# Kernel optimization log

Hardware: AMD Instinct MI355X
Metric: run time of the kernel (lower is better)

Reference implementation:

```python
import jax, jax.numpy as jnp
import numpy as np
import math

DIM = 1024
NUM_HEADS = 16
HEAD_DIM = DIM // NUM_HEADS
SCALE = HEAD_DIM ** -0.5
WINDOW_SIZE = 256
IS_SLIDING = True
IS_CAUSAL = True


def _alibi_slopes(num_heads: int) -> np.ndarray:
    closest_pow2 = 2 ** math.floor(math.log2(num_heads))
    base = 2.0 ** (-2.0 ** (-(math.log2(closest_pow2) - 3)))
    powers = np.arange(1, closest_pow2 + 1, dtype=np.float32)
    slopes = base ** powers
    if num_heads != closest_pow2:
        start = 2.0 ** (-(2.0 ** (-(math.log2(closest_pow2) - 3)) - 1))
        extra = np.linspace(start, base, num_heads - closest_pow2, dtype=np.float32)
        slopes = np.concatenate([slopes, extra])
    return slopes.astype(np.float32)


def setup_inputs() -> dict:
    key = jax.random.key(0)
    k_x, k_qw, k_qb, k_pw, k_pb = jax.random.split(key, 5)
    B, N, C = 2, 2048, DIM
    s = C ** -0.5
    return {
        "x": jax.random.normal(k_x, (B, N, C), dtype=jnp.float32),
        "qkv_w": jax.random.normal(k_qw, (3 * C, C), dtype=jnp.float32) * s,
        "qkv_b": jax.random.normal(k_qb, (3 * C,), dtype=jnp.float32) * 0.02,
        "proj_w": jax.random.normal(k_pw, (C, C), dtype=jnp.float32) * s,
        "proj_b": jax.random.normal(k_pb, (C,), dtype=jnp.float32) * 0.02,
    }


def reference(x, qkv_w, qkv_b, proj_w, proj_b):
    B, N, C = x.shape
    H, D = NUM_HEADS, HEAD_DIM
    slopes = jnp.asarray(_alibi_slopes(H))  # [H]

    qkv = x @ qkv_w.T + qkv_b                         # [B,N,3C]
    qkv = qkv.reshape(B, N, 3, H, D).transpose(2, 0, 3, 1, 4)  # [3,B,H,N,D]
    q, k, v = qkv[0], qkv[1], qkv[2]

    attn = jnp.einsum('bhnd,bhmd->bhnm', q, k) * SCALE  # [B,H,N,N]

    pos = jnp.arange(N)
    rel = pos[None, :] - pos[:, None]                  # rel[i,j] = j - i
    # alibi = slope*|rel|, negated where rel<0  ==  slope*rel
    alibi = slopes[:, None, None] * rel.astype(jnp.float32)   # [H,N,N]
    attn = attn + alibi[None]

    if IS_SLIDING:
        attn = jnp.where(jnp.abs(rel) >= WINDOW_SIZE, -jnp.inf, attn)
    if IS_CAUSAL:
        attn = jnp.where(rel > 0, -jnp.inf, attn)      # mask strictly-upper triangle

    attn = jax.nn.softmax(attn, axis=-1)
    out = jnp.einsum('bhnm,bhmd->bhnd', attn, v)       # [B,H,N,D]
    out = out.transpose(0, 2, 1, 3).reshape(B, N, C)
    return out @ proj_w.T + proj_b
```

## Files before the change

### kernel.cpp

```cpp
#include <hip/hip_runtime.h>
#include <hip/hip_bf16.h>
#include <cmath>

#define B_ 2
#define N_ 2048
#define C_ 1024
#define H_ 16
#define D_ 64
#define BHND (B_*H_*N_*D_)

typedef __attribute__((ext_vector_type(8))) short  bf16x8;
typedef __attribute__((ext_vector_type(4))) float  f32x4;
typedef __attribute__((ext_vector_type(4))) unsigned int uint4v;
typedef __attribute__((ext_vector_type(2))) unsigned int uint2v;

__device__ __forceinline__ unsigned pack_hi2(float x0, float x1) {
  return __builtin_amdgcn_perm(__float_as_uint(x1), __float_as_uint(x0), 0x07060302u);
}
__device__ __forceinline__ float trunc16(float x) {
  return __uint_as_float(__float_as_uint(x) & 0xFFFF0000u);
}
__device__ __forceinline__ void cvt8(const float4 u, const float4 v,
                                     uint4v& hi, uint4v& lo) {
  hi.x = pack_hi2(u.x, u.y); hi.y = pack_hi2(u.z, u.w);
  hi.z = pack_hi2(v.x, v.y); hi.w = pack_hi2(v.z, v.w);
  float l0 = u.x - trunc16(u.x), l1 = u.y - trunc16(u.y);
  float l2 = u.z - trunc16(u.z), l3 = u.w - trunc16(u.w);
  float l4 = v.x - trunc16(v.x), l5 = v.y - trunc16(v.y);
  float l6 = v.z - trunc16(v.z), l7 = v.w - trunc16(v.w);
  lo.x = pack_hi2(l0, l1); lo.y = pack_hi2(l2, l3);
  lo.z = pack_hi2(l4, l5); lo.w = pack_hi2(l6, l7);
}
__device__ __forceinline__ int swz(int row, int kelem) {
  return ((row << 7) + (kelem << 1)) ^ ((row & 7) << 4);
}

template<int MODE>
__global__ __launch_bounds__(256, 2)
void gemm3_nt(const float* __restrict__ A, const float* __restrict__ Bw,
              const float* __restrict__ bias, float* __restrict__ Cd,
              int Ncols, int K)
{
  __shared__ char smem[65536];
  char* Ah = smem;          char* Al = smem + 16384;
  char* Bh = smem + 32768;  char* Bl = smem + 49152;

  const int t    = threadIdx.x;
  const int lane = t & 63;
  const int w    = t >> 6;
  const int wm   = w >> 1, wn = w & 1;
  const int mb   = blockIdx.x, nb = blockIdx.y;

  const int srow = t >> 1;
  const int skh  = (t & 1) * 32;
  const float* Ag = A  + (size_t)(mb*128 + srow)*K + skh;
  const float* Bg = Bw + (size_t)(nb*128 + srow)*K + skh;

  f32x4 acc[4][4];
  #pragma unroll
  for (int m = 0; m < 4; ++m)
    #pragma unroll
    for (int n = 0; n < 4; ++n) acc[m][n] = (f32x4)0.f;

  float4 fa[8], fb[8];
  {
    const float4* ap = (const float4*)Ag;
    const float4* bp = (const float4*)Bg;
    #pragma unroll
    for (int i = 0; i < 8; ++i) { fa[i] = ap[i]; fb[i] = bp[i]; }
  }

  const int fr = lane & 15;
  const int fg = lane >> 4;
  const int nkt = K / 64;

  for (int kt = 0; kt < nkt; ++kt) {
    __syncthreads();
    #pragma unroll
    for (int cc = 0; cc < 4; ++cc) {
      uint4v hi, lo;
      const int off = swz(srow, skh + cc*8);
      cvt8(fa[2*cc], fa[2*cc+1], hi, lo);
      *(uint4v*)(Ah + off) = hi;  *(uint4v*)(Al + off) = lo;
      cvt8(fb[2*cc], fb[2*cc+1], hi, lo);
      *(uint4v*)(Bh + off) = hi;  *(uint4v*)(Bl + off) = lo;
    }
    __syncthreads();
    if (kt + 1 < nkt) {
      const float4* ap = (const float4*)(Ag + (kt+1)*64);
      const float4* bp = (const float4*)(Bg + (kt+1)*64);
      #pragma unroll
      for (int i = 0; i < 8; ++i) { fa[i] = ap[i]; fb[i] = bp[i]; }
    }
    #pragma unroll
    for (int ks = 0; ks < 2; ++ks) {
      const int ke = ks*32 + fg*8;
      bf16x8 ah[4], al[4];
      #pragma unroll
      for (int m = 0; m < 4; ++m) {
        const int off = swz(wm*64 + m*16 + fr, ke);
        ah[m] = *(const bf16x8*)(Ah + off);
        al[m] = *(const bf16x8*)(Al + off);
      }
      #pragma unroll
      for (int n = 0; n < 4; ++n) {
        const int off = swz(wn*64 + n*16 + fr, ke);
        const bf16x8 bh = *(const bf16x8*)(Bh + off);
        const bf16x8 bl = *(const bf16x8*)(Bl + off);
        #pragma unroll
        for (int m = 0; m < 4; ++m) {
          acc[m][n] = __builtin_amdgcn_mfma_f32_16x16x32_bf16(ah[m], bh, acc[m][n], 0, 0, 0);
          acc[m][n] = __builtin_amdgcn_mfma_f32_16x16x32_bf16(al[m], bh, acc[m][n], 0, 0, 0);
          acc[m][n] = __builtin_amdgcn_mfma_f32_16x16x32_bf16(ah[m], bl, acc[m][n], 0, 0, 0);
        }
      }
    }
  }

  #pragma unroll
  for (int n = 0; n < 4; ++n) {
    const int col = nb*128 + wn*64 + n*16 + fr;
    const float bb = bias[col];
    int which = 0, hh = 0, dd = 0;
    if (MODE == 1) { which = col >> 10; hh = (col >> 6) & 15; dd = col & 63; }
    #pragma unroll
    for (int m = 0; m < 4; ++m) {
      const int row0 = mb*128 + wm*64 + m*16 + fg*4;
      #pragma unroll
      for (int j = 0; j < 4; ++j) {
        const int row = row0 + j;
        const float val = acc[m][n][j] + bb;
        if (MODE == 0) {
          Cd[(size_t)row*Ncols + col] = val;
        } else {
          const int b = row >> 11, i = row & 2047;
          Cd[(size_t)which*BHND + (((size_t)(b*H_ + hh))*N_ + i)*D_ + dd] = val;
        }
      }
    }
  }
}

__global__ __launch_bounds__(256, 2)
void attn_mfma(const float* __restrict__ qkv, float* __restrict__ attn_out)
{
  __shared__ char smem[65536];
  char* Qh = smem;
  char* Ql = smem + 8192;
  char* Kh = smem + 16384;
  char* Kl = smem + 24576;
  char* Vh = smem + 32768;
  char* Vl = smem + 40960;
  char* Ph = smem + 49152;
  char* Pl = smem + 57344;

  const int t    = threadIdx.x;
  const int lane = t & 63;
  const int w    = t >> 6;
  const int g    = lane >> 4;
  const int c    = lane & 15;
  const int qt   = blockIdx.x & 31;
  const int bh   = blockIdx.x >> 5;
  const int h    = bh & 15;
  const int b    = bh >> 4;

  const float* qg = qkv + (size_t)bh*N_*D_;
  const float* kg = qg + (size_t)BHND;
  const float* vg = kg + (size_t)BHND;

  const float slope = exp2f(-0.5f*(float)(h+1));
  const int kt0 = max(0, qt - 4);
  const int ktN = qt;

  const int srow = t >> 2;
  const int scq  = (t & 3) * 16;
  const int vkey = t & 63;
  const int vdb  = (t >> 6) * 16;

  {
    const float4* qp = (const float4*)(qg + (size_t)(qt*64 + srow)*D_ + scq);
    float4 q0=qp[0], q1=qp[1], q2=qp[2], q3=qp[3];
    const float4* kp = (const float4*)(kg + (size_t)(kt0*64 + srow)*D_ + scq);
    float4 k0=kp[0], k1=kp[1], k2=kp[2], k3=kp[3];
    const float4* vp = (const float4*)(vg + (size_t)(kt0*64 + vkey)*D_ + vdb);
    float4 v0=vp[0], v1=vp[1], v2=vp[2], v3=vp[3];
    uint4v hi, lo;
    cvt8(q0,q1,hi,lo); *(uint4v*)(Qh+swz(srow,scq  ))=hi; *(uint4v*)(Ql+swz(srow,scq  ))=lo;
    cvt8(q2,q3,hi,lo); *(uint4v*)(Qh+swz(srow,scq+8))=hi; *(uint4v*)(Ql+swz(srow,scq+8))=lo;
    cvt8(k0,k1,hi,lo); *(uint4v*)(Kh+swz(srow,scq  ))=hi; *(uint4v*)(Kl+swz(srow,scq  ))=lo;
    cvt8(k2,k3,hi,lo); *(uint4v*)(Kh+swz(srow,scq+8))=hi; *(uint4v*)(Kl+swz(srow,scq+8))=lo;
    const float vv[16] = {v0.x,v0.y,v0.z,v0.w, v1.x,v1.y,v1.z,v1.w,
                          v2.x,v2.y,v2.z,v2.w, v3.x,v3.y,v3.z,v3.w};
    #pragma unroll
    for (int d16 = 0; d16 < 16; ++d16) {
      const int d  = vdb + d16;
      const int off = swz(d, vkey);
      const unsigned xu = __float_as_uint(vv[d16]);
      *(unsigned short*)(Vh + off) = (unsigned short)(xu >> 16);
      const float xt = __uint_as_float(xu & 0xFFFF0000u);
      *(unsigned short*)(Vl + off) = (unsigned short)(__float_as_uint(vv[d16] - xt) >> 16);
    }
  }
  __syncthreads();

  bf16x8 qbh[2], qbl[2];
  #pragma unroll
  for (int ks = 0; ks < 2; ++ks) {
    const int off = swz(w*16 + c, ks*32 + g*8);
    qbh[ks] = *(const bf16x8*)(Qh + off);
    qbl[ks] = *(const bf16x8*)(Ql + off);
  }

  float4 pk[4], pvv[4];
  if (kt0 < ktN) {
    const float4* kp = (const float4*)(kg + (size_t)((kt0+1)*64 + srow)*D_ + scq);
    const float4* vp = (const float4*)(vg + (size_t)((kt0+1)*64 + vkey)*D_ + vdb);
    #pragma unroll
    for (int i = 0; i < 4; ++i) { pk[i] = kp[i]; pvv[i] = vp[i]; }
  }

  f32x4 co[4];
  #pragma unroll
  for (int n = 0; n < 4; ++n) co[n] = (f32x4)0.f;
  float mrun = -1e20f, lrun = 0.f;
  const int iq = qt*64 + w*16 + c;
  const int pbase = w*2048;

  for (int kt = kt0; ; ++kt) {
    f32x4 sc[4];
    #pragma unroll
    for (int f = 0; f < 4; ++f) sc[f] = (f32x4)0.f;
    #pragma unroll
    for (int ks = 0; ks < 2; ++ks) {
      #pragma unroll
      for (int f = 0; f < 4; ++f) {
        const int off = swz(f*16 + c, ks*32 + g*8);
        const bf16x8 ah = *(const bf16x8*)(Kh + off);
        const bf16x8 al = *(const bf16x8*)(Kl + off);
        sc[f] = __builtin_amdgcn_mfma_f32_16x16x32_bf16(ah, qbh[ks], sc[f], 0,0,0);
        sc[f] = __builtin_amdgcn_mfma_f32_16x16x32_bf16(al, qbh[ks], sc[f], 0,0,0);
        sc[f] = __builtin_amdgcn_mfma_f32_16x16x32_bf16(ah, qbl[ks], sc[f], 0,0,0);
      }
    }
    float sv[4][4];
    float mt = -1e30f;
    #pragma unroll
    for (int f = 0; f < 4; ++f)
      #pragma unroll
      for (int r = 0; r < 4; ++r) {
        const int rel = kt*64 + f*16 + g*4 + r - iq;
        float s = fmaf(sc[f][r], 0.125f, slope*(float)rel);
        s = (rel > 0 || rel < -255) ? -1e30f : s;
        sv[f][r] = s;
        mt = fmaxf(mt, s);
      }
    mt = fmaxf(mt, __shfl_xor(mt, 16));
    mt = fmaxf(mt, __shfl_xor(mt, 32));
    const float mnew = fmaxf(mrun, mt);
    const float corr = __expf(mrun - mnew);
    mrun = mnew;
    float pw[4][4];
    float psum = 0.f;
    #pragma unroll
    for (int f = 0; f < 4; ++f)
      #pragma unroll
      for (int r = 0; r < 4; ++r) {
        const float p = __expf(sv[f][r] - mnew);
        pw[f][r] = p;
        psum += p;
      }
    psum += __shfl_xor(psum, 16);
    psum += __shfl_xor(psum, 32);
    lrun = lrun*corr + psum;
    #pragma unroll
    for (int f = 0; f < 4; ++f) {
      const int off = swz(c, f*16 + g*4);
      uint2v ph2, pl2;
      ph2.x = pack_hi2(pw[f][0], pw[f][1]);
      ph2.y = pack_hi2(pw[f][2], pw[f][3]);
      pl2.x = pack_hi2(pw[f][0]-trunc16(pw[f][0]), pw[f][1]-trunc16(pw[f][1]));
      pl2.y = pack_hi2(pw[f][2]-trunc16(pw[f][2]), pw[f][3]-trunc16(pw[f][3]));
      *(uint2v*)(Ph + pbase + off) = ph2;
      *(uint2v*)(Pl + pbase + off) = pl2;
    }
    const float c0 = __shfl(corr, g*4+0);
    const float c1 = __shfl(corr, g*4+1);
    const float c2 = __shfl(corr, g*4+2);
    const float c3 = __shfl(corr, g*4+3);
    #pragma unroll
    for (int n = 0; n < 4; ++n) {
      co[n][0] *= c0; co[n][1] *= c1; co[n][2] *= c2; co[n][3] *= c3;
    }
    #pragma unroll
    for (int ks = 0; ks < 2; ++ks) {
      const int poff = swz(c, ks*32 + g*8);
      const bf16x8 pah = *(const bf16x8*)(Ph + pbase + poff);
      const bf16x8 pal = *(const bf16x8*)(Pl + pbase + poff);
      #pragma unroll
      for (int n = 0; n < 4; ++n) {
        const int voff = swz(n*16 + c, ks*32 + g*8);
        const bf16x8 vbh = *(const bf16x8*)(Vh + voff);
        const bf16x8 vbl = *(const bf16x8*)(Vl + voff);
        co[n] = __builtin_amdgcn_mfma_f32_16x16x32_bf16(pah, vbh, co[n], 0,0,0);
        co[n] = __builtin_amdgcn_mfma_f32_16x16x32_bf16(pal, vbh, co[n], 0,0,0);
        co[n] = __builtin_amdgcn_mfma_f32_16x16x32_bf16(pah, vbl, co[n], 0,0,0);
      }
    }
    if (kt == ktN) break;
    __syncthreads();
    {
      uint4v hi, lo;
      cvt8(pk[0], pk[1], hi, lo);
      *(uint4v*)(Kh+swz(srow,scq  ))=hi; *(uint4v*)(Kl+swz(srow,scq  ))=lo;
      cvt8(pk[2], pk[3], hi, lo);
      *(uint4v*)(Kh+swz(srow,scq+8))=hi; *(uint4v*)(Kl+swz(srow,scq+8))=lo;
      const float vv[16] = {pvv[0].x,pvv[0].y,pvv[0].z,pvv[0].w,
                            pvv[1].x,pvv[1].y,pvv[1].z,pvv[1].w,
                            pvv[2].x,pvv[2].y,pvv[2].z,pvv[2].w,
                            pvv[3].x,pvv[3].y,pvv[3].z,pvv[3].w};
      #pragma unroll
      for (int d16 = 0; d16 < 16; ++d16) {
        const int d  = vdb + d16;
        const int off = swz(d, vkey);
        const unsigned xu = __float_as_uint(vv[d16]);
        *(unsigned short*)(Vh + off) = (unsigned short)(xu >> 16);
        const float xt = __uint_as_float(xu & 0xFFFF0000u);
        *(unsigned short*)(Vl + off) = (unsigned short)(__float_as_uint(vv[d16] - xt) >> 16);
      }
    }
    __syncthreads();
    if (kt + 1 < ktN) {
      const float4* kp = (const float4*)(kg + (size_t)((kt+2)*64 + srow)*D_ + scq);
      const float4* vp = (const float4*)(vg + (size_t)((kt+2)*64 + vkey)*D_ + vdb);
      #pragma unroll
      for (int i = 0; i < 4; ++i) { pk[i] = kp[i]; pvv[i] = vp[i]; }
    }
  }

  float linv[4];
  #pragma unroll
  for (int r = 0; r < 4; ++r) linv[r] = 1.f / __shfl(lrun, g*4+r);
  #pragma unroll
  for (int n = 0; n < 4; ++n)
    #pragma unroll
    for (int r = 0; r < 4; ++r) {
      const int qrow = qt*64 + w*16 + g*4 + r;
      attn_out[((size_t)b*N_ + qrow)*C_ + h*64 + n*16 + c] = co[n][r] * linv[r];
    }
}

extern "C" void kernel_launch(void* const* d_in, const int* in_sizes, int n_in,
                              void* d_out, int out_size, void* d_ws, size_t ws_size,
                              hipStream_t stream)
{
  const float* x      = (const float*)d_in[0];
  const float* qkv_w  = (const float*)d_in[1];
  const float* qkv_b  = (const float*)d_in[2];
  const float* proj_w = (const float*)d_in[3];
  const float* proj_b = (const float*)d_in[4];
  float* out  = (float*)d_out;
  float* qkv  = (float*)d_ws;
  float* attn = qkv + (size_t)3*BHND;

  gemm3_nt<1><<<dim3(32, 24), 256, 0, stream>>>(x, qkv_w, qkv_b, qkv, 3*C_, C_);
  attn_mfma<<<dim3(1024), 256, 0, stream>>>(qkv, attn);
  gemm3_nt<0><<<dim3(32, 8), 256, 0, stream>>>(attn, proj_w, proj_b, out, C_, C_);
}
```

Baseline: 285.5 us.

## Pre-split fp32 operands into bf16 hi/lo planes in global memory between stages

Adds a conversion kernel that splits x and both weight matrices into separate bf16 high and low arrays. The GEMM and attention kernels now load these pre-split arrays directly instead of converting fp32 on every tile load. The QKV projection and attention epilogues now also write split hi/lo bf16 outputs. This removes repeated in-kernel conversion work and keeps the total byte count per element the same, at the cost of three extra launches and extra passes over x and the weights. The new path only runs if the workspace is at least about 96 MiB; otherwise the old fp32 path is used.

```diff
diff --git a/kernel.cpp b/kernel.cpp
--- a/kernel.cpp
+++ b/kernel.cpp
@@ -8,11 +8,13 @@
 #define H_ 16
 #define D_ 64
 #define BHND (B_*H_*N_*D_)
+#define BNC  (B_*N_*C_)
 
 typedef __attribute__((ext_vector_type(8))) short  bf16x8;
 typedef __attribute__((ext_vector_type(4))) float  f32x4;
 typedef __attribute__((ext_vector_type(4))) unsigned int uint4v;
 typedef __attribute__((ext_vector_type(2))) unsigned int uint2v;
+typedef unsigned short ushort_t;
 
 __device__ __forceinline__ unsigned pack_hi2(float x0, float x1) {
   return __builtin_amdgcn_perm(__float_as_uint(x1), __float_as_uint(x0), 0x07060302u);
@@ -35,11 +37,29 @@
   return ((row << 7) + (kelem << 1)) ^ ((row & 7) << 4);
 }
 
+
+__global__ __launch_bounds__(256)
+void cvt_split(const float* __restrict__ in, ushort_t* __restrict__ h,
+               ushort_t* __restrict__ l, int n4)
+{
+  for (int i = blockIdx.x*256 + threadIdx.x; i < n4; i += gridDim.x*256) {
+    const float4 v = ((const float4*)in)[i];
+    uint2v hh, ll;
+    hh.x = pack_hi2(v.x, v.y); hh.y = pack_hi2(v.z, v.w);
+    ll.x = pack_hi2(v.x - trunc16(v.x), v.y - trunc16(v.y));
+    ll.y = pack_hi2(v.z - trunc16(v.z), v.w - trunc16(v.w));
+    *(uint2v*)(h + 4*(size_t)i) = hh;
+    *(uint2v*)(l + 4*(size_t)i) = ll;
+  }
+}
+
 template<int MODE>
 __global__ __launch_bounds__(256, 2)
-void gemm3_nt(const float* __restrict__ A, const float* __restrict__ Bw,
-              const float* __restrict__ bias, float* __restrict__ Cd,
-              int Ncols, int K)
+void gemm_b3(const ushort_t* __restrict__ Agh_, const ushort_t* __restrict__ Agl_,
+             const ushort_t* __restrict__ Bgh_, const ushort_t* __restrict__ Bgl_,
+             const float* __restrict__ bias, float* __restrict__ Cf,
+             ushort_t* __restrict__ Ch, ushort_t* __restrict__ Cl,
+             int Ncols, int K)
 {
   __shared__ char smem[65536];
   char* Ah = smem;          char* Al = smem + 16384;
@@ -53,8 +73,10 @@
 
   const int srow = t >> 1;
   const int skh  = (t & 1) * 32;
-  const float* Ag = A  + (size_t)(mb*128 + srow)*K + skh;
-  const float* Bg = Bw + (size_t)(nb*128 + srow)*K + skh;
+  const ushort_t* Agh = Agh_ + (size_t)(mb*128 + srow)*K + skh;
+  const ushort_t* Agl = Agl_ + (size_t)(mb*128 + srow)*K + skh;
+  const ushort_t* Bgh = Bgh_ + (size_t)(nb*128 + srow)*K + skh;
+  const ushort_t* Bgl = Bgl_ + (size_t)(nb*128 + srow)*K + skh;
 
   f32x4 acc[4][4];
   #pragma unroll
@@ -62,12 +84,13 @@
     #pragma unroll
     for (int n = 0; n < 4; ++n) acc[m][n] = (f32x4)0.f;
 
-  float4 fa[8], fb[8];
-  {
-    const float4* ap = (const float4*)Ag;
-    const float4* bp = (const float4*)Bg;
-    #pragma unroll
-    for (int i = 0; i < 8; ++i) { fa[i] = ap[i]; fb[i] = bp[i]; }
+  uint4v fah[4], fal[4], fbh[4], fbl[4];
+  #pragma unroll
+  for (int i = 0; i < 4; ++i) {
+    fah[i] = *(const uint4v*)(Agh + i*8);
+    fal[i] = *(const uint4v*)(Agl + i*8);
+    fbh[i] = *(const uint4v*)(Bgh + i*8);
+    fbl[i] = *(const uint4v*)(Bgl + i*8);
   }
 
   const int fr = lane & 15;
@@ -78,19 +101,20 @@
     __syncthreads();
     #pragma unroll
     for (int cc = 0; cc < 4; ++cc) {
-      uint4v hi, lo;
       const int off = swz(srow, skh + cc*8);
-      cvt8(fa[2*cc], fa[2*cc+1], hi, lo);
-      *(uint4v*)(Ah + off) = hi;  *(uint4v*)(Al + off) = lo;
-      cvt8(fb[2*cc], fb[2*cc+1], hi, lo);
-      *(uint4v*)(Bh + off) = hi;  *(uint4v*)(Bl + off) = lo;
+      *(uint4v*)(Ah + off) = fah[cc];  *(uint4v*)(Al + off) = fal[cc];
+      *(uint4v*)(Bh + off) = fbh[cc];  *(uint4v*)(Bl + off) = fbl[cc];
     }
     __syncthreads();
     if (kt + 1 < nkt) {
-      const float4* ap = (const float4*)(Ag + (kt+1)*64);
-      const float4* bp = (const float4*)(Bg + (kt+1)*64);
-      #pragma unroll
-      for (int i = 0; i < 8; ++i) { fa[i] = ap[i]; fb[i] = bp[i]; }
+      const int ko = (kt+1)*64;
+      #pragma unroll
+      for (int i = 0; i < 4; ++i) {
+        fah[i] = *(const uint4v*)(Agh + ko + i*8);
+        fal[i] = *(const uint4v*)(Agl + ko + i*8);
+        fbh[i] = *(const uint4v*)(Bgh + ko + i*8);
+        fbl[i] = *(const uint4v*)(Bgl + ko + i*8);
+      }
     }
     #pragma unroll
     for (int ks = 0; ks < 2; ++ks) {
@@ -117,6 +141,329 @@
     }
   }
 
+  #pragma unroll
+  for (int n = 0; n < 4; ++n) {
+    const int col = nb*128 + wn*64 + n*16 + fr;
+    const float bb = bias[col];
+    int which = 0, hh = 0, dd = 0;
+    if (MODE == 1) { which = col >> 10; hh = (col >> 6) & 15; dd = col & 63; }
+    #pragma unroll
+    for (int m = 0; m < 4; ++m) {
+      const int row0 = mb*128 + wm*64 + m*16 + fg*4;
+      #pragma unroll
+      for (int j = 0; j < 4; ++j) {
+        const int row = row0 + j;
+        const float val = acc[m][n][j] + bb;
+        if (MODE == 0) {
+          Cf[(size_t)row*Ncols + col] = val;
+        } else {
+          const int b = row >> 11, i = row & 2047;
+          const size_t idx = (size_t)which*BHND + (((size_t)(b*H_ + hh))*N_ + i)*D_ + dd;
+          Ch[idx] = (ushort_t)(__float_as_uint(val) >> 16);
+          Cl[idx] = (ushort_t)(__float_as_uint(val - trunc16(val)) >> 16);
+        }
+      }
+    }
+  }
+}
+
+__global__ __launch_bounds__(256, 2)
+void attn_b3(const ushort_t* __restrict__ qkvh, const ushort_t* __restrict__ qkvl,
+             ushort_t* __restrict__ outh, ushort_t* __restrict__ outl)
+{
+  __shared__ char smem[65536];
+  char* Qh = smem;
+  char* Ql = smem + 8192;
+  char* Kh = smem + 16384;
+  char* Kl = smem + 24576;
+  char* Vh = smem + 32768;
+  char* Vl = smem + 40960;
+  char* Ph = smem + 49152;
+  char* Pl = smem + 57344;
+
+  const int t    = threadIdx.x;
+  const int lane = t & 63;
+  const int w    = t >> 6;
+  const int g    = lane >> 4;
+  const int c    = lane & 15;
+  const int qt   = blockIdx.x & 31;
+  const int bh   = blockIdx.x >> 5;
+  const int h    = bh & 15;
+  const int b    = bh >> 4;
+
+  const ushort_t* qgh = qkvh + (size_t)bh*N_*D_;
+  const ushort_t* qgl = qkvl + (size_t)bh*N_*D_;
+  const ushort_t* kgh = qkvh + (size_t)BHND   + (size_t)bh*N_*D_;
+  const ushort_t* kgl = qkvl + (size_t)BHND   + (size_t)bh*N_*D_;
+  const ushort_t* vgh = qkvh + (size_t)2*BHND + (size_t)bh*N_*D_;
+  const ushort_t* vgl = qkvl + (size_t)2*BHND + (size_t)bh*N_*D_;
+
+  const float slope = exp2f(-0.5f*(float)(h+1));
+  const int kt0 = max(0, qt - 4);
+  const int ktN = qt;
+
+  const int srow = t >> 2;
+  const int scq  = (t & 3) * 16;
+  const int vkey = t & 63;
+  const int vdb  = (t >> 6) * 16;
+
+  {
+    const uint4v* qph = (const uint4v*)(qgh + (size_t)(qt*64 + srow)*D_ + scq);
+    const uint4v* qpl = (const uint4v*)(qgl + (size_t)(qt*64 + srow)*D_ + scq);
+    const uint4v* kph = (const uint4v*)(kgh + (size_t)(kt0*64 + srow)*D_ + scq);
+    const uint4v* kpl = (const uint4v*)(kgl + (size_t)(kt0*64 + srow)*D_ + scq);
+    const uint4v* vph = (const uint4v*)(vgh + (size_t)(kt0*64 + vkey)*D_ + vdb);
+    const uint4v* vpl = (const uint4v*)(vgl + (size_t)(kt0*64 + vkey)*D_ + vdb);
+    uint4v q0=qph[0], q1=qph[1], ql0=qpl[0], ql1=qpl[1];
+    uint4v k0=kph[0], k1=kph[1], kl0=kpl[0], kl1=kpl[1];
+    uint4v v0=vph[0], v1=vph[1], vl0=vpl[0], vl1=vpl[1];
+    *(uint4v*)(Qh+swz(srow,scq))   = q0;  *(uint4v*)(Qh+swz(srow,scq+8)) = q1;
+    *(uint4v*)(Ql+swz(srow,scq))   = ql0; *(uint4v*)(Ql+swz(srow,scq+8)) = ql1;
+    *(uint4v*)(Kh+swz(srow,scq))   = k0;  *(uint4v*)(Kh+swz(srow,scq+8)) = k1;
+    *(uint4v*)(Kl+swz(srow,scq))   = kl0; *(uint4v*)(Kl+swz(srow,scq+8)) = kl1;
+    #pragma unroll
+    for (int j = 0; j < 4; ++j) {
+      const int d0 = vdb + 2*j, d1 = vdb + 8 + 2*j;
+      unsigned wh = v0[j], wl = vl0[j];
+      *(ushort_t*)(Vh + swz(d0,   vkey)) = (ushort_t)(wh & 0xffffu);
+      *(ushort_t*)(Vh + swz(d0+1, vkey)) = (ushort_t)(wh >> 16);
+      *(ushort_t*)(Vl + swz(d0,   vkey)) = (ushort_t)(wl & 0xffffu);
+      *(ushort_t*)(Vl + swz(d0+1, vkey)) = (ushort_t)(wl >> 16);
+      wh = v1[j]; wl = vl1[j];
+      *(ushort_t*)(Vh + swz(d1,   vkey)) = (ushort_t)(wh & 0xffffu);
+      *(ushort_t*)(Vh + swz(d1+1, vkey)) = (ushort_t)(wh >> 16);
+      *(ushort_t*)(Vl + swz(d1,   vkey)) = (ushort_t)(wl & 0xffffu);
+      *(ushort_t*)(Vl + swz(d1+1, vkey)) = (ushort_t)(wl >> 16);
+    }
+  }
+  __syncthreads();
+
+  bf16x8 qbh[2], qbl[2];
+  #pragma unroll
+  for (int ks = 0; ks < 2; ++ks) {
+    const int off = swz(w*16 + c, ks*32 + g*8);
+    qbh[ks] = *(const bf16x8*)(Qh + off);
+    qbl[ks] = *(const bf16x8*)(Ql + off);
+  }
+
+  uint4v pkh[2], pkl[2], pvh[2], pvl[2];
+  if (kt0 < ktN) {
+    const uint4v* kph = (const uint4v*)(kgh + (size_t)((kt0+1)*64 + srow)*D_ + scq);
+    const uint4v* kpl = (const uint4v*)(kgl + (size_t)((kt0+1)*64 + srow)*D_ + scq);
+    const uint4v* vph = (const uint4v*)(vgh + (size_t)((kt0+1)*64 + vkey)*D_ + vdb);
+    const uint4v* vpl = (const uint4v*)(vgl + (size_t)((kt0+1)*64 + vkey)*D_ + vdb);
+    pkh[0]=kph[0]; pkh[1]=kph[1]; pkl[0]=kpl[0]; pkl[1]=kpl[1];
+    pvh[0]=vph[0]; pvh[1]=vph[1]; pvl[0]=vpl[0]; pvl[1]=vpl[1];
+  }
+
+  f32x4 co[4];
+  #pragma unroll
+  for (int n = 0; n < 4; ++n) co[n] = (f32x4)0.f;
+  float mrun = -1e20f, lrun = 0.f;
+  const int iq = qt*64 + w*16 + c;
+  const int pbase = w*2048;
+
+  for (int kt = kt0; ; ++kt) {
+    f32x4 sc[4];
+    #pragma unroll
+    for (int f = 0; f < 4; ++f) sc[f] = (f32x4)0.f;
+    #pragma unroll
+    for (int ks = 0; ks < 2; ++ks) {
+      #pragma unroll
+      for (int f = 0; f < 4; ++f) {
+        const int off = swz(f*16 + c, ks*32 + g*8);
+        const bf16x8 ah = *(const bf16x8*)(Kh + off);
+        const bf16x8 al = *(const bf16x8*)(Kl + off);
+        sc[f] = __builtin_amdgcn_mfma_f32_16x16x32_bf16(ah, qbh[ks], sc[f], 0,0,0);
+        sc[f] = __builtin_amdgcn_mfma_f32_16x16x32_bf16(al, qbh[ks], sc[f], 0,0,0);
+        sc[f] = __builtin_amdgcn_mfma_f32_16x16x32_bf16(ah, qbl[ks], sc[f], 0,0,0);
+      }
+    }
+    float sv[4][4];
+    float mt = -1e30f;
+    #pragma unroll
+    for (int f = 0; f < 4; ++f)
+      #pragma unroll
+      for (int r = 0; r < 4; ++r) {
+        const int rel = kt*64 + f*16 + g*4 + r - iq;
+        float s = fmaf(sc[f][r], 0.125f, slope*(float)rel);
+        s = (rel > 0 || rel < -255) ? -1e30f : s;
+        sv[f][r] = s;
+        mt = fmaxf(mt, s);
+      }
+    mt = fmaxf(mt, __shfl_xor(mt, 16));
+    mt = fmaxf(mt, __shfl_xor(mt, 32));
+    const float mnew = fmaxf(mrun, mt);
+    const float corr = __expf(mrun - mnew);
+    mrun = mnew;
+    float pw[4][4];
+    float psum = 0.f;
+    #pragma unroll
+    for (int f = 0; f < 4; ++f)
+      #pragma unroll
+      for (int r = 0; r < 4; ++r) {
+        const float p = __expf(sv[f][r] - mnew);
+        pw[f][r] = p;
+        psum += p;
+      }
+    psum += __shfl_xor(psum, 16);
+    psum += __shfl_xor(psum, 32);
+    lrun = lrun*corr + psum;
+    #pragma unroll
+    for (int f = 0; f < 4; ++f) {
+      const int off = swz(c, f*16 + g*4);
+      uint2v ph2, pl2;
+      ph2.x = pack_hi2(pw[f][0], pw[f][1]);
+      ph2.y = pack_hi2(pw[f][2], pw[f][3]);
+      pl2.x = pack_hi2(pw[f][0]-trunc16(pw[f][0]), pw[f][1]-trunc16(pw[f][1]));
+      pl2.y = pack_hi2(pw[f][2]-trunc16(pw[f][2]), pw[f][3]-trunc16(pw[f][3]));
+      *(uint2v*)(Ph + pbase + off) = ph2;
+      *(uint2v*)(Pl + pbase + off) = pl2;
+    }
+    const float c0 = __shfl(corr, g*4+0);
+    const float c1 = __shfl(corr, g*4+1);
+    const float c2 = __shfl(corr, g*4+2);
+    const float c3 = __shfl(corr, g*4+3);
+    #pragma unroll
+    for (int n = 0; n < 4; ++n) {
+      co[n][0] *= c0; co[n][1] *= c1; co[n][2] *= c2; co[n][3] *= c3;
+    }
+    #pragma unroll
+    for (int ks = 0; ks < 2; ++ks) {
+      const int poff = swz(c, ks*32 + g*8);
+      const bf16x8 pah = *(const bf16x8*)(Ph + pbase + poff);
+      const bf16x8 pal = *(const bf16x8*)(Pl + pbase + poff);
+      #pragma unroll
+      for (int n = 0; n < 4; ++n) {
+        const int voff = swz(n*16 + c, ks*32 + g*8);
+        const bf16x8 vbh = *(const bf16x8*)(Vh + voff);
+        const bf16x8 vbl = *(const bf16x8*)(Vl + voff);
+        co[n] = __builtin_amdgcn_mfma_f32_16x16x32_bf16(pah, vbh, co[n], 0,0,0);
+        co[n] = __builtin_amdgcn_mfma_f32_16x16x32_bf16(pal, vbh, co[n], 0,0,0);
+        co[n] = __builtin_amdgcn_mfma_f32_16x16x32_bf16(pah, vbl, co[n], 0,0,0);
+      }
+    }
+    if (kt == ktN) break;
+    __syncthreads();
+    {
+      *(uint4v*)(Kh+swz(srow,scq))   = pkh[0]; *(uint4v*)(Kh+swz(srow,scq+8)) = pkh[1];
+      *(uint4v*)(Kl+swz(srow,scq))   = pkl[0]; *(uint4v*)(Kl+swz(srow,scq+8)) = pkl[1];
+      #pragma unroll
+      for (int j = 0; j < 4; ++j) {
+        const int d0 = vdb + 2*j, d1 = vdb + 8 + 2*j;
+        unsigned wh = pvh[0][j], wl = pvl[0][j];
+        *(ushort_t*)(Vh + swz(d0,   vkey)) = (ushort_t)(wh & 0xffffu);
+        *(ushort_t*)(Vh + swz(d0+1, vkey)) = (ushort_t)(wh >> 16);
+        *(ushort_t*)(Vl + swz(d0,   vkey)) = (ushort_t)(wl & 0xffffu);
+        *(ushort_t*)(Vl + swz(d0+1, vkey)) = (ushort_t)(wl >> 16);
+        wh = pvh[1][j]; wl = pvl[1][j];
+        *(ushort_t*)(Vh + swz(d1,   vkey)) = (ushort_t)(wh & 0xffffu);
+        *(ushort_t*)(Vh + swz(d1+1, vkey)) = (ushort_t)(wh >> 16);
+        *(ushort_t*)(Vl + swz(d1,   vkey)) = (ushort_t)(wl & 0xffffu);
+        *(ushort_t*)(Vl + swz(d1+1, vkey)) = (ushort_t)(wl >> 16);
+      }
+    }
+    __syncthreads();
+    if (kt + 1 < ktN) {
+      const uint4v* kph = (const uint4v*)(kgh + (size_t)((kt+2)*64 + srow)*D_ + scq);
+      const uint4v* kpl = (const uint4v*)(kgl + (size_t)((kt+2)*64 + srow)*D_ + scq);
+      const uint4v* vph = (const uint4v*)(vgh + (size_t)((kt+2)*64 + vkey)*D_ + vdb);
+      const uint4v* vpl = (const uint4v*)(vgl + (size_t)((kt+2)*64 + vkey)*D_ + vdb);
+      pkh[0]=kph[0]; pkh[1]=kph[1]; pkl[0]=kpl[0]; pkl[1]=kpl[1];
+      pvh[0]=vph[0]; pvh[1]=vph[1]; pvl[0]=vpl[0]; pvl[1]=vpl[1];
+    }
+  }
+
+  float linv[4];
+  #pragma unroll
+  for (int r = 0; r < 4; ++r) linv[r] = 1.f / __shfl(lrun, g*4+r);
+  #pragma unroll
+  for (int n = 0; n < 4; ++n)
+    #pragma unroll
+    for (int r = 0; r < 4; ++r) {
+      const int qrow = qt*64 + w*16 + g*4 + r;
+      const float val = co[n][r] * linv[r];
+      const size_t idx = ((size_t)b*N_ + qrow)*C_ + h*64 + n*16 + c;
+      outh[idx] = (ushort_t)(__float_as_uint(val) >> 16);
+      outl[idx] = (ushort_t)(__float_as_uint(val - trunc16(val)) >> 16);
+    }
+}
+
+template<int MODE>
+__global__ __launch_bounds__(256, 2)
+void gemm3_nt(const float* __restrict__ A, const float* __restrict__ Bw,
+              const float* __restrict__ bias, float* __restrict__ Cd,
+              int Ncols, int K)
+{
+  __shared__ char smem[65536];
+  char* Ah = smem;          char* Al = smem + 16384;
+  char* Bh = smem + 32768;  char* Bl = smem + 49152;
+  const int t = threadIdx.x;
+  const int lane = t & 63;
+  const int w = t >> 6;
+  const int wm = w >> 1, wn = w & 1;
+  const int mb = blockIdx.x, nb = blockIdx.y;
+  const int srow = t >> 1;
+  const int skh  = (t & 1) * 32;
+  const float* Ag = A  + (size_t)(mb*128 + srow)*K + skh;
+  const float* Bg = Bw + (size_t)(nb*128 + srow)*K + skh;
+  f32x4 acc[4][4];
+  #pragma unroll
+  for (int m = 0; m < 4; ++m)
+    #pragma unroll
+    for (int n = 0; n < 4; ++n) acc[m][n] = (f32x4)0.f;
+  float4 fa[8], fb[8];
+  {
+    const float4* ap = (const float4*)Ag;
+    const float4* bp = (const float4*)Bg;
+    #pragma unroll
+    for (int i = 0; i < 8; ++i) { fa[i] = ap[i]; fb[i] = bp[i]; }
+  }
+  const int fr = lane & 15;
+  const int fg = lane >> 4;
+  const int nkt = K / 64;
+  for (int kt = 0; kt < nkt; ++kt) {
+    __syncthreads();
+    #pragma unroll
+    for (int cc = 0; cc < 4; ++cc) {
+      uint4v hi, lo;
+      const int off = swz(srow, skh + cc*8);
+      cvt8(fa[2*cc], fa[2*cc+1], hi, lo);
+      *(uint4v*)(Ah + off) = hi;  *(uint4v*)(Al + off) = lo;
+      cvt8(fb[2*cc], fb[2*cc+1], hi, lo);
+      *(uint4v*)(Bh + off) = hi;  *(uint4v*)(Bl + off) = lo;
+    }
+    __syncthreads();
+    if (kt + 1 < nkt) {
+      const float4* ap = (const float4*)(Ag + (kt+1)*64);
+      const float4* bp = (const float4*)(Bg + (kt+1)*64);
+      #pragma unroll
+      for (int i = 0; i < 8; ++i) { fa[i] = ap[i]; fb[i] = bp[i]; }
+    }
+    #pragma unroll
+    for (int ks = 0; ks < 2; ++ks) {
+      const int ke = ks*32 + fg*8;
+      bf16x8 ah[4], al[4];
+      #pragma unroll
+      for (int m = 0; m < 4; ++m) {
+        const int off = swz(wm*64 + m*16 + fr, ke);
+        ah[m] = *(const bf16x8*)(Ah + off);
+        al[m] = *(const bf16x8*)(Al + off);
+      }
+      #pragma unroll
+      for (int n = 0; n < 4; ++n) {
+        const int off = swz(wn*64 + n*16 + fr, ke);
+        const bf16x8 bh = *(const bf16x8*)(Bh + off);
+        const bf16x8 bl = *(const bf16x8*)(Bl + off);
+        #pragma unroll
+        for (int m = 0; m < 4; ++m) {
+          acc[m][n] = __builtin_amdgcn_mfma_f32_16x16x32_bf16(ah[m], bh, acc[m][n], 0, 0, 0);
+          acc[m][n] = __builtin_amdgcn_mfma_f32_16x16x32_bf16(al[m], bh, acc[m][n], 0, 0, 0);
+          acc[m][n] = __builtin_amdgcn_mfma_f32_16x16x32_bf16(ah[m], bl, acc[m][n], 0, 0, 0);
+        }
+      }
+    }
+  }
   #pragma unroll
   for (int n = 0; n < 4; ++n) {
     const int col = nb*128 + wn*64 + n*16 + fr;
@@ -153,30 +500,25 @@
   char* Vl = smem + 40960;
   char* Ph = smem + 49152;
   char* Pl = smem + 57344;
-
-  const int t    = threadIdx.x;
+  const int t = threadIdx.x;
   const int lane = t & 63;
-  const int w    = t >> 6;
-  const int g    = lane >> 4;
-  const int c    = lane & 15;
-  const int qt   = blockIdx.x & 31;
-  const int bh   = blockIdx.x >> 5;
-  const int h    = bh & 15;
-  const int b    = bh >> 4;
-
+  const int w = t >> 6;
+  const int g = lane >> 4;
+  const int c = lane & 15;
+  const int qt = blockIdx.x & 31;
+  const int bh = blockIdx.x >> 5;
+  const int h = bh & 15;
+  const int b = bh >> 4;
   const float* qg = qkv + (size_t)bh*N_*D_;
   const float* kg = qg + (size_t)BHND;
   const float* vg = kg + (size_t)BHND;
-
   const float slope = exp2f(-0.5f*(float)(h+1));
   const int kt0 = max(0, qt - 4);
   const int ktN = qt;
-
   const int srow = t >> 2;
   const int scq  = (t & 3) * 16;
   const int vkey = t & 63;
   const int vdb  = (t >> 6) * 16;
-
   {
     const float4* qp = (const float4*)(qg + (size_t)(qt*64 + srow)*D_ + scq);
     float4 q0=qp[0], q1=qp[1], q2=qp[2], q3=qp[3];
@@ -202,7 +544,6 @@
     }
   }
   __syncthreads();
-
   bf16x8 qbh[2], qbl[2];
   #pragma unroll
   for (int ks = 0; ks < 2; ++ks) {
@@ -210,7 +551,6 @@
     qbh[ks] = *(const bf16x8*)(Qh + off);
     qbl[ks] = *(const bf16x8*)(Ql + off);
   }
-
   float4 pk[4], pvv[4];
   if (kt0 < ktN) {
     const float4* kp = (const float4*)(kg + (size_t)((kt0+1)*64 + srow)*D_ + scq);
@@ -218,14 +558,12 @@
     #pragma unroll
     for (int i = 0; i < 4; ++i) { pk[i] = kp[i]; pvv[i] = vp[i]; }
   }
-
   f32x4 co[4];
   #pragma unroll
   for (int n = 0; n < 4; ++n) co[n] = (f32x4)0.f;
   float mrun = -1e20f, lrun = 0.f;
   const int iq = qt*64 + w*16 + c;
   const int pbase = w*2048;
-
   for (int kt = kt0; ; ++kt) {
     f32x4 sc[4];
     #pragma unroll
@@ -336,7 +674,6 @@
       for (int i = 0; i < 4; ++i) { pk[i] = kp[i]; pvv[i] = vp[i]; }
     }
   }
-
   float linv[4];
   #pragma unroll
   for (int r = 0; r < 4; ++r) linv[r] = 1.f / __shfl(lrun, g*4+r);
@@ -358,11 +695,36 @@
   const float* qkv_b  = (const float*)d_in[2];
   const float* proj_w = (const float*)d_in[3];
   const float* proj_b = (const float*)d_in[4];
-  float* out  = (float*)d_out;
-  float* qkv  = (float*)d_ws;
-  float* attn = qkv + (size_t)3*BHND;
-
-  gemm3_nt<1><<<dim3(32, 24), 256, 0, stream>>>(x, qkv_w, qkv_b, qkv, 3*C_, C_);
-  attn_mfma<<<dim3(1024), 256, 0, stream>>>(qkv, attn);
-  gemm3_nt<0><<<dim3(32, 8), 256, 0, stream>>>(attn, proj_w, proj_b, out, C_, C_);
-}
+  float* out = (float*)d_out;
+
+  const size_t NEED = 100663296;
+  if (ws_size >= NEED) {
+    ushort_t* W     = (ushort_t*)d_ws;
+    ushort_t* qkvh  = W;
+    ushort_t* qkvl  = qkvh + (size_t)3*BHND;
+    ushort_t* attnh = qkvl + (size_t)3*BHND;
+    ushort_t* attnl = attnh + (size_t)BNC;
+    ushort_t* xh    = attnl + (size_t)BNC;
+    ushort_t* xl    = xh + (size_t)BNC;
+    ushort_t* qwh   = xl + (size_t)BNC;
+    ushort_t* qwl   = qwh + (size_t)3*C_*C_;
+    ushort_t* pwh   = qwl + (size_t)3*C_*C_;
+    ushort_t* pwl   = pwh + (size_t)C_*C_;
+
+    auto grid_for = [](int n4) { int g = (n4 + 255) / 256; return g > 2048 ? 2048 : g; };
+    cvt_split<<<grid_for(BNC/4), 256, 0, stream>>>(x, xh, xl, BNC/4);
+    cvt_split<<<grid_for(3*C_*C_/4), 256, 0, stream>>>(qkv_w, qwh, qwl, 3*C_*C_/4);
+    cvt_split<<<grid_for(C_*C_/4), 256, 0, stream>>>(proj_w, pwh, pwl, C_*C_/4);
+    gemm_b3<1><<<dim3(32, 24), 256, 0, stream>>>(xh, xl, qwh, qwl, qkv_b,
+                                                 nullptr, qkvh, qkvl, 3*C_, C_);
+    attn_b3<<<dim3(1024), 256, 0, stream>>>(qkvh, qkvl, attnh, attnl);
+    gemm_b3<0><<<dim3(32, 8), 256, 0, stream>>>(attnh, attnl, pwh, pwl, proj_b,
+                                                out, nullptr, nullptr, C_, C_);
+  } else {
+    float* qkv  = (float*)d_ws;
+    float* attn = qkv + (size_t)3*BHND;
+    gemm3_nt<1><<<dim3(32, 24), 256, 0, stream>>>(x, qkv_w, qkv_b, qkv, 3*C_, C_);
+    attn_mfma<<<dim3(1024), 256, 0, stream>>>(qkv, attn);
+    gemm3_nt<0><<<dim3(32, 8), 256, 0, stream>>>(attn, proj_w, proj_b, out, C_, C_);
+  }
+}
```

Measured after the change: 242.0 us. 1.18x faster.
